# Performance work log

Hardware: AMD Instinct MI355X
Metric: run time of the kernel (lower is better)

Reference implementation:

```python
import math
import jax, jax.numpy as jnp
import numpy as np

D_MODEL = 1024
NUM_HEADS = 16
MAX_SEQ_LEN = 2048
THETA = 10000.0


def setup_inputs() -> dict:
    key = jax.random.key(0)
    ks = jax.random.split(key, 5)
    B, S, D = 2, 2048, D_MODEL
    std = math.sqrt(2.0 / (D + D))
    x = jax.random.normal(ks[0], (B, S, D), dtype=jnp.float32)
    wq = jax.random.normal(ks[1], (D, D), dtype=jnp.float32) * std
    wk = jax.random.normal(ks[2], (D, D), dtype=jnp.float32) * std
    wv = jax.random.normal(ks[3], (D, D), dtype=jnp.float32) * std
    wo = jax.random.normal(ks[4], (D, D), dtype=jnp.float32) * std
    return {"x": x, "wq": wq, "wk": wk, "wv": wv, "wo": wo}


def _rope_tables(seq_len: int, d_k: int):
    # angles[i, k] = i / theta^(2k/d_k), k over d_k//2 pairs
    inv_freq = 1.0 / (THETA ** (jnp.arange(0, d_k, 2, dtype=jnp.float32) / d_k))
    angles = jnp.arange(seq_len, dtype=jnp.float32)[:, None] * inv_freq[None, :]  # [S, d_k/2]
    return jnp.cos(angles), jnp.sin(angles)


def _apply_rope(x, cos, sin):
    # x: [..., S, d_k]; cos/sin: [S, d_k/2], broadcast over leading dims
    x_even = x[..., ::2]
    x_odd = x[..., 1::2]
    r_even = x_even * cos - x_odd * sin
    r_odd = x_even * sin + x_odd * cos
    return jnp.stack([r_even, r_odd], axis=-1).reshape(x.shape)


def reference(x, wq, wk, wv, wo):
    B, S, D = x.shape
    H = NUM_HEADS
    dk = D // H

    def split_heads(t):  # [B,S,D] -> [B,H,S,dk]
        return t.reshape(B, S, H, dk).transpose(0, 2, 1, 3)

    Q = split_heads(x @ wq.T)
    K = split_heads(x @ wk.T)
    V = split_heads(x @ wv.T)

    cos, sin = _rope_tables(S, dk)
    Q = _apply_rope(Q, cos, sin)
    K = _apply_rope(K, cos, sin)

    scores = jnp.einsum('bhqd,bhkd->bhqk', Q, K) / jnp.sqrt(jnp.float32(dk))
    mask = jnp.tril(jnp.ones((S, S), dtype=bool))  # causal: q can attend k <= q
    neg_inf = jnp.float32(-jnp.inf)
    scores = jnp.where(mask, scores, neg_inf)
    m = jnp.max(scores, axis=-1, keepdims=True)
    m = jnp.where(jnp.isinf(m), jnp.zeros_like(m), m)
    exp_scores = jnp.exp(scores - m)
    exp_scores = jnp.where(mask, exp_scores, 0.0)
    attn = exp_scores / (jnp.sum(exp_scores, axis=-1, keepdims=True) + 1e-9)
    out = jnp.einsum('bhqk,bhkd->bhqd', attn, V)  # [B,H,S,dk]
    out = out.transpose(0, 2, 1, 3).reshape(B, S, D)
    return out @ wo.T
```

## Files before the change

### kernel.cpp

```cpp
#include <hip/hip_runtime.h>
#include <stdint.h>

typedef unsigned short u16;
typedef unsigned int u32;
typedef __bf16 bf16x8 __attribute__((ext_vector_type(8)));
typedef float f32x4 __attribute__((ext_vector_type(4)));
typedef unsigned short u16x8 __attribute__((ext_vector_type(8)));

#define D_MODEL 1024
#define SEQ 2048
#define NH 16
#define DK 64
#define NROWS 4096

static __device__ __forceinline__ u16 f2bf(float f) {
  u32 u = __float_as_uint(f);
  u = (u + 0x7FFFu + ((u >> 16) & 1u)) >> 16;
  return (u16)u;
}
static __device__ __forceinline__ float bf2f(u16 h) {
  return __uint_as_float(((u32)h) << 16);
}
static __device__ __forceinline__ f32x4 mfma16(bf16x8 a, bf16x8 b, f32x4 c) {
  return __builtin_amdgcn_mfma_f32_16x16x32_bf16(a, b, c, 0, 0, 0);
}
static __device__ __forceinline__ void gload16(const void* g, void* l) {
  __builtin_amdgcn_global_load_lds(
      (const __attribute__((address_space(1))) void*)g,
      (__attribute__((address_space(3))) void*)l, 16, 0, 0);
}

static __device__ __forceinline__ float xor32_max(float x) {
#if __has_builtin(__builtin_amdgcn_permlane32_swap)
  u32 a = __float_as_uint(x), b = a;
  auto pr = __builtin_amdgcn_permlane32_swap(a, b, false, false);
  return fmaxf(__uint_as_float(pr[0]), __uint_as_float(pr[1]));
#else
  return fmaxf(x, __shfl_xor(x, 32));
#endif
}
static __device__ __forceinline__ float xor32_add(float x) {
#if __has_builtin(__builtin_amdgcn_permlane32_swap)
  u32 a = __float_as_uint(x), b = a;
  auto pr = __builtin_amdgcn_permlane32_swap(a, b, false, false);
  return __uint_as_float(pr[0]) + __uint_as_float(pr[1]);
#else
  return x + __shfl_xor(x, 32);
#endif
}

__global__ __launch_bounds__(256) void k_cast(
    const float* __restrict__ x, const float* __restrict__ wq,
    const float* __restrict__ wk, const float* __restrict__ wv,
    const float* __restrict__ wo, u16* __restrict__ xb, u16* __restrict__ wqb,
    u16* __restrict__ wkb, u16* __restrict__ wvb, u16* __restrict__ wob) {
  size_t e = ((size_t)blockIdx.x * 256 + threadIdx.x) * 8;
  const float* s;
  u16* d;
  size_t off;
  if (e < (size_t)NROWS * D_MODEL) {
    s = x; d = xb; off = e;
  } else {
    size_t r = e - (size_t)NROWS * D_MODEL;
    unsigned wi = (unsigned)(r >> 20);
    off = r & 1048575u;
    s = wi == 0 ? wq : wi == 1 ? wk : wi == 2 ? wv : wo;
    d = wi == 0 ? wqb : wi == 1 ? wkb : wi == 2 ? wvb : wob;
  }
  float4 a = *(const float4*)(s + off);
  float4 b = *(const float4*)(s + off + 4);
  u16x8 o;
  o[0] = f2bf(a.x); o[1] = f2bf(a.y); o[2] = f2bf(a.z); o[3] = f2bf(a.w);
  o[4] = f2bf(b.x); o[5] = f2bf(b.y); o[6] = f2bf(b.z); o[7] = f2bf(b.w);
  *(u16x8*)(d + off) = o;
}

__global__ __launch_bounds__(256) void k_tab(float* __restrict__ ct, float* __restrict__ st) {
  int i = blockIdx.x * 256 + threadIdx.x;
  int s = i >> 5, p = i & 31;
  double ang = (double)s * pow(10000.0, -(double)p / 32.0);
  ct[i] = (float)cos(ang);
  st[i] = (float)sin(ang);
}

template <bool MULTI, bool OUTF32>
__global__ __launch_bounds__(256, 1) void k_gemm(
    const u16* __restrict__ A, const u16* __restrict__ B0,
    const u16* __restrict__ B1, const u16* __restrict__ B2,
    u16* __restrict__ Cb, float* __restrict__ Cf, int ldc) {
  constexpr int K = 1024;
  const int mb = blockIdx.x, nb = blockIdx.y;
  const int tid = threadIdx.x;
  const int lane = tid & 63, w = tid >> 6;
  const int lq = lane & 15, lg = lane >> 4;
  const int wm = w >> 1, wn = w & 1;
  __shared__ __align__(16) u16 As[128 * 32];
  __shared__ __align__(16) u16 Bs[128 * 32];

  const u16* Bp;
  if (MULTI) {
    int sel = nb >> 3;
    Bp = sel == 0 ? B0 : (sel == 1 ? B1 : B2);
  } else {
    Bp = B0;
  }
  int nloc = MULTI ? (nb & 7) * 128 : nb * 128;
  const char* Ab = (const char*)A + (size_t)mb * 128 * 2048;
  const char* Bb = (const char*)Bp + (size_t)nloc * 2048;

  const int srow = tid >> 2;
  const int scb = (tid & 3) * 16;

  f32x4 zero4 = {0.f, 0.f, 0.f, 0.f};
  f32x4 acc[4][4];
#pragma unroll
  for (int i = 0; i < 4; ++i)
#pragma unroll
    for (int j = 0; j < 4; ++j) acc[i][j] = zero4;

  for (int k0 = 0; k0 < K; k0 += 32) {
#pragma unroll
    for (int c = 0; c < 2; ++c) {
      int o = c * 4096 + tid * 16;
      const char* ga = Ab + (size_t)(c * 64 + srow) * 2048 + k0 * 2 + scb;
      const char* gb = Bb + (size_t)(c * 64 + srow) * 2048 + k0 * 2 + scb;
      gload16(ga, (char*)As + o);
      gload16(gb, (char*)Bs + o);
    }
    __syncthreads();
    bf16x8 af[4], bfr[4];
#pragma unroll
    for (int i = 0; i < 4; ++i) {
      af[i] = *(const bf16x8*)((const char*)As + (wm * 64 + i * 16 + lq) * 64 + lg * 16);
      bfr[i] = *(const bf16x8*)((const char*)Bs + (wn * 64 + i * 16 + lq) * 64 + lg * 16);
    }
#pragma unroll
    for (int i = 0; i < 4; ++i)
#pragma unroll
      for (int j = 0; j < 4; ++j) acc[i][j] = mfma16(af[i], bfr[j], acc[i][j]);
    __syncthreads();
  }

#pragma unroll
  for (int i = 0; i < 4; ++i) {
#pragma unroll
    for (int r = 0; r < 4; ++r) {
      size_t rowg = (size_t)(mb * 128 + wm * 64 + i * 16 + lg * 4 + r);
#pragma unroll
      for (int j = 0; j < 4; ++j) {
        int colg = nb * 128 + wn * 64 + j * 16 + lq;
        if (OUTF32)
          Cf[rowg * ldc + colg] = acc[i][j][r];
        else
          Cb[rowg * ldc + colg] = f2bf(acc[i][j][r]);
      }
    }
  }
}

__global__ __launch_bounds__(256) void k_rope(const u16* __restrict__ qkv,
                                              const float* __restrict__ ct,
                                              const float* __restrict__ st,
                                              u16* __restrict__ qh, u16* __restrict__ kh) {
  int gi = blockIdx.x * 256 + threadIdx.x;
  int row = gi >> 7;
  int col = (gi & 127) << 3;
  int h = col >> 6, d0 = col & 63;
  int b = row >> 11, s = row & 2047;
  const int srcoff = blockIdx.y ? 1024 : 0;
  const float qs = blockIdx.y ? 1.0f : 0.18033688011112042f;
  u16x8 v = *(const u16x8*)(qkv + (size_t)row * 3072 + srcoff + col);
  const float* cp = ct + s * 32 + (d0 >> 1);
  const float* sp = st + s * 32 + (d0 >> 1);
  u16x8 o;
#pragma unroll
  for (int i = 0; i < 4; ++i) {
    float ev = bf2f(v[2 * i]), od = bf2f(v[2 * i + 1]);
    float c = cp[i], sn = sp[i];
    o[2 * i] = f2bf((ev * c - od * sn) * qs);
    o[2 * i + 1] = f2bf((ev * sn + od * c) * qs);
  }
  u16* dst = blockIdx.y ? kh : qh;
  *(u16x8*)(dst + (((size_t)(b * 16 + h) * SEQ + s) << 6) + d0) = o;
}

__global__ __launch_bounds__(256) void k_vtrans(const u16* __restrict__ qkv,
                                                u16* __restrict__ vt) {
  __shared__ __align__(16) u16 t[64][72];
  int sb = blockIdx.x, bh = blockIdx.y;
  int b = bh >> 4, h = bh & 15;
  int tid = threadIdx.x;
#pragma unroll
  for (int c = 0; c < 2; ++c) {
    int o = tid * 8 + c * 2048;
    int r = o >> 6, d = o & 63;
    u16x8 v = *(const u16x8*)(qkv + (size_t)(b * SEQ + sb * 64 + r) * 3072 + 2048 + h * 64 + d);
    *(u16x8*)&t[r][d] = v;
  }
  __syncthreads();
#pragma unroll
  for (int c = 0; c < 2; ++c) {
    int o = tid * 8 + c * 2048;
    int d = o >> 6, si = o & 63;
    u16x8 v;
#pragma unroll
    for (int j = 0; j < 8; ++j) v[j] = t[si + j][d];
    *(u16x8*)(vt + ((size_t)bh * 64 + d) * SEQ + sb * 64 + si) = v;
  }
}

static __device__ __forceinline__ void attn_tile(
    const u16* Kl, const u16* Vl, u16* Plw, int k0, int qrow, int lq, int lg,
    bf16x8 qf0, bf16x8 qf1, float& m_run, float& l_run, f32x4* accO, bool masked) {
  f32x4 zero4 = {0.f, 0.f, 0.f, 0.f};
  f32x4 sa[4];
  sa[0] = zero4; sa[1] = zero4; sa[2] = zero4; sa[3] = zero4;
  __builtin_amdgcn_s_setprio(1);
#pragma unroll
  for (int kt = 0; kt < 4; ++kt) {
    int krow = kt * 16 + lq;
    int base = krow * 128 + lg * 16;
    int swz = (krow & 7) << 4;
    bf16x8 kf0 = *(const bf16x8*)((const char*)Kl + (base ^ swz));
    bf16x8 kf1 = *(const bf16x8*)((const char*)Kl + ((base + 64) ^ swz));
    sa[kt] = mfma16(kf0, qf0, sa[kt]);
    sa[kt] = mfma16(kf1, qf1, sa[kt]);
  }
  __builtin_amdgcn_s_setprio(0);

  float p[16];
#pragma unroll
  for (int kt = 0; kt < 4; ++kt)
#pragma unroll
    for (int r = 0; r < 4; ++r) p[kt * 4 + r] = sa[kt][r];
  if (masked) {
#pragma unroll
    for (int kt = 0; kt < 4; ++kt)
#pragma unroll
      for (int r = 0; r < 4; ++r) {
        int key = k0 + kt * 16 + lg * 4 + r;
        if (key > qrow) p[kt * 4 + r] = -1e30f;
      }
  }
  float x0 = fmaxf(p[0], p[1]), x1 = fmaxf(p[2], p[3]);
  float x2 = fmaxf(p[4], p[5]), x3 = fmaxf(p[6], p[7]);
  float x4 = fmaxf(p[8], p[9]), x5 = fmaxf(p[10], p[11]);
  float x6 = fmaxf(p[12], p[13]), x7 = fmaxf(p[14], p[15]);
  x0 = fmaxf(x0, x1); x2 = fmaxf(x2, x3); x4 = fmaxf(x4, x5); x6 = fmaxf(x6, x7);
  x0 = fmaxf(x0, x2); x4 = fmaxf(x4, x6);
  float pm = fmaxf(x0, x4);
  pm = fmaxf(pm, __shfl_xor(pm, 16));
  pm = xor32_max(pm);
  const bool resc = __any(pm > m_run + 8.0f);
  float mnew = resc ? fmaxf(m_run, pm) : m_run;
#pragma unroll
  for (int i = 0; i < 16; ++i) p[i] = __builtin_amdgcn_exp2f(p[i] - mnew);
  float s0 = p[0] + p[1], s1 = p[2] + p[3], s2 = p[4] + p[5], s3 = p[6] + p[7];
  float s4 = p[8] + p[9], s5 = p[10] + p[11], s6 = p[12] + p[13], s7 = p[14] + p[15];
  s0 += s1; s2 += s3; s4 += s5; s6 += s7;
  s0 += s2; s4 += s6;
  float rs = s0 + s4;
  rs += __shfl_xor(rs, 16);
  rs = xor32_add(rs);
  if (resc) {
    float alpha = __builtin_amdgcn_exp2f(m_run - mnew);
    l_run = l_run * alpha + rs;
    m_run = mnew;
#pragma unroll
    for (int r = 0; r < 4; ++r) {
      float ar = __shfl(alpha, lg * 4 + r);
#pragma unroll
      for (int dt = 0; dt < 4; ++dt) accO[dt][r] *= ar;
    }
  } else {
    l_run += rs;
  }

  {
    int swz = (lq & 7) << 4;
#pragma unroll
    for (int kt = 0; kt < 4; ++kt) {
      u32 w0, w1;
      asm("v_cvt_pk_bf16_f32 %0, %1, %2"
          : "=v"(w0) : "v"(p[kt * 4 + 0]), "v"(p[kt * 4 + 1]));
      asm("v_cvt_pk_bf16_f32 %0, %1, %2"
          : "=v"(w1) : "v"(p[kt * 4 + 2]), "v"(p[kt * 4 + 3]));
      int a0 = (lq * 128 + (kt * 16 + lg * 4) * 2) ^ swz;
      int a1 = (lq * 128 + (kt * 16 + lg * 4 + 2) * 2) ^ swz;
      *(u32*)((char*)Plw + a0) = w0;
      *(u32*)((char*)Plw + a1) = w1;
    }
  }
  {
    int swz = (lq & 7) << 4;
    bf16x8 pa0 = *(const bf16x8*)((const char*)Plw + ((lq * 128 + lg * 16) ^ swz));
    bf16x8 pa1 = *(const bf16x8*)((const char*)Plw + ((lq * 128 + 64 + lg * 16) ^ swz));
    __builtin_amdgcn_s_setprio(1);
#pragma unroll
    for (int dt = 0; dt < 4; ++dt) {
      int vrow = dt * 16 + lq;
      int vb = vrow * 128 + lg * 16;
      int vs = (vrow & 7) << 4;
      bf16x8 v0 = *(const bf16x8*)((const char*)Vl + (vb ^ vs));
      bf16x8 v1 = *(const bf16x8*)((const char*)Vl + ((vb + 64) ^ vs));
      accO[dt] = mfma16(pa0, v0, accO[dt]);
      accO[dt] = mfma16(pa1, v1, accO[dt]);
    }
    __builtin_amdgcn_s_setprio(0);
  }
}

__global__ __launch_bounds__(512, 2) void k_attn(const u16* __restrict__ qh,
                                                 const u16* __restrict__ kh,
                                                 const u16* __restrict__ vt,
                                                 u16* __restrict__ ao) {
  const int qb1 = (int)blockIdx.x;
  const int qb2 = 15 - qb1;
  const int bh = blockIdx.y;
  const int tid = threadIdx.x;
  const int w = tid >> 6;
  const int lane = tid & 63;
  const int lq = lane & 15;
  const int lg = lane >> 4;

  __shared__ __align__(16) u16 Kd[2][64 * 64];
  __shared__ __align__(16) u16 Vd[2][64 * 64];
  __shared__ __align__(16) u16 Pl[8][16 * 64];

  const int qtop1 = qb1 * 128 + w * 16;
  const int qtop2 = qb2 * 128 + w * 16;
  const int qrow1 = qtop1 + lq;
  const int qrow2 = qtop2 + lq;

  const u16* qp1 = qh + ((size_t)bh * SEQ + qrow1) * DK + lg * 8;
  const u16* qp2 = qh + ((size_t)bh * SEQ + qrow2) * DK + lg * 8;
  bf16x8 qa0 = *(const bf16x8*)qp1;
  bf16x8 qa1 = *(const bf16x8*)(qp1 + 32);
  bf16x8 qb0 = *(const bf16x8*)qp2;
  bf16x8 qb1f = *(const bf16x8*)(qp2 + 32);

  f32x4 zero4 = {0.f, 0.f, 0.f, 0.f};
  f32x4 acc1[4], acc2[4];
#pragma unroll
  for (int dt = 0; dt < 4; ++dt) { acc1[dt] = zero4; acc2[dt] = zero4; }
  float m1 = -1e30f, l1 = 0.f, m2 = -1e30f, l2 = 0.f;

  const int NT = 2 * qb2 + 2;
  const int nt1 = 2 * qb1 + (w >> 2) + 1;
  const int nt2 = 2 * qb2 + (w >> 2) + 1;

  const int srow = tid >> 3;
  const int scb = (tid & 7) * 16;
  const int colb = scb ^ ((srow & 7) << 4);
  const char* kbase = (const char*)(kh + ((size_t)bh * SEQ + srow) * DK) + colb;
  const char* vbase = (const char*)(vt + ((size_t)bh * DK + srow) * SEQ) + colb;

  gload16(kbase, (char*)Kd[0] + tid * 16);
  gload16(vbase, (char*)Vd[0] + tid * 16);
  __syncthreads();

  for (int t = 0; t < NT; ++t) {
    const int cur = t & 1;
    if (t + 1 < NT) {
      gload16(kbase + (size_t)(t + 1) * 8192, (char*)Kd[cur ^ 1] + tid * 16);
      gload16(vbase + (size_t)(t + 1) * 128, (char*)Vd[cur ^ 1] + tid * 16);
    }
    const int k0 = t * 64;
    if (t < nt1)
      attn_tile(Kd[cur], Vd[cur], Pl[w], k0, qrow1, lq, lg, qa0, qa1, m1, l1,
                acc1, t == nt1 - 1);
    if (t < nt2)
      attn_tile(Kd[cur], Vd[cur], Pl[w], k0, qrow2, lq, lg, qb0, qb1f, m2, l2,
                acc2, t == nt2 - 1);
    __syncthreads();
  }

  const int b = bh >> 4, h = bh & 15;
#pragma unroll
  for (int r = 0; r < 4; ++r) {
    float lr = __shfl(l1, lg * 4 + r);
    float inv = 1.f / (lr + 1e-9f);
    int qq = qtop1 + lg * 4 + r;
    u16* orow = ao + ((size_t)b * SEQ + qq) * D_MODEL + h * DK;
#pragma unroll
    for (int dt = 0; dt < 4; ++dt) orow[dt * 16 + lq] = f2bf(acc1[dt][r] * inv);
  }
#pragma unroll
  for (int r = 0; r < 4; ++r) {
    float lr = __shfl(l2, lg * 4 + r);
    float inv = 1.f / (lr + 1e-9f);
    int qq = qtop2 + lg * 4 + r;
    u16* orow = ao + ((size_t)b * SEQ + qq) * D_MODEL + h * DK;
#pragma unroll
    for (int dt = 0; dt < 4; ++dt) orow[dt * 16 + lq] = f2bf(acc2[dt][r] * inv);
  }
}

extern "C" void kernel_launch(void* const* d_in, const int* in_sizes, int n_in,
                              void* d_out, int out_size, void* d_ws, size_t ws_size,
                              hipStream_t stream) {
  const float* x = (const float*)d_in[0];
  const float* wq = (const float*)d_in[1];
  const float* wk = (const float*)d_in[2];
  const float* wv = (const float*)d_in[3];
  const float* wo = (const float*)d_in[4];
  float* out = (float*)d_out;
  char* ws = (char*)d_ws;

  u16* xb   = (u16*)(ws + 0);
  u16* wqb  = (u16*)(ws + 8388608);
  u16* wkb  = (u16*)(ws + 10485760);
  u16* wvb  = (u16*)(ws + 12582912);
  u16* wob  = (u16*)(ws + 14680064);
  u16* qkv  = (u16*)(ws + 16777216);
  u16* qhb  = (u16*)(ws + 41943040);
  u16* khb  = (u16*)(ws + 50331648);
  u16* vtb  = (u16*)(ws + 58720256);
  u16* aob  = (u16*)(ws + 67108864);
  float* ct = (float*)(ws + 75497472);
  float* st = (float*)(ws + 75759616);

  k_cast<<<4096, 256, 0, stream>>>(x, wq, wk, wv, wo, xb, wqb, wkb, wvb, wob);
  k_tab<<<256, 256, 0, stream>>>(ct, st);
  k_gemm<true, false><<<dim3(32, 24), 256, 0, stream>>>(xb, wqb, wkb, wvb, qkv, nullptr, 3072);
  k_rope<<<dim3(2048, 2), 256, 0, stream>>>(qkv, ct, st, qhb, khb);
  k_vtrans<<<dim3(32, 32), 256, 0, stream>>>(qkv, vtb);
  k_attn<<<dim3(8, 32), 512, 0, stream>>>(qhb, khb, vtb, aob);
  k_gemm<false, true><<<dim3(32, 8), 256, 0, stream>>>(aob, wob, nullptr, nullptr, nullptr, out, 1024);
}
```

Baseline: 132.6 us.

## Shrink attention blocks to 64 query rows and stage two KV tiles per sync

The attention kernel now uses 256-thread blocks of four waves, each block covering two 64-row query tiles paired for causal load balance. The grid doubles to 16x32 blocks. Each loop iteration double-buffers and loads two 64-key K/V tiles, halving the number of __syncthreads per key range. The goal is more blocks for better CU occupancy and balance, and less barrier overhead. In exchange, K/V are loaded from global memory by more blocks, and per-block LDS use grows to about 72 KB.

```diff
diff --git a/kernel.cpp b/kernel.cpp
--- a/kernel.cpp
+++ b/kernel.cpp
@@ -310,12 +310,12 @@
   }
 }
 
-__global__ __launch_bounds__(512, 2) void k_attn(const u16* __restrict__ qh,
+__global__ __launch_bounds__(256, 2) void k_attn(const u16* __restrict__ qh,
                                                  const u16* __restrict__ kh,
                                                  const u16* __restrict__ vt,
                                                  u16* __restrict__ ao) {
   const int qb1 = (int)blockIdx.x;
-  const int qb2 = 15 - qb1;
+  const int qb2 = 31 - qb1;
   const int bh = blockIdx.y;
   const int tid = threadIdx.x;
   const int w = tid >> 6;
@@ -323,12 +323,12 @@
   const int lq = lane & 15;
   const int lg = lane >> 4;
 
-  __shared__ __align__(16) u16 Kd[2][64 * 64];
-  __shared__ __align__(16) u16 Vd[2][64 * 64];
-  __shared__ __align__(16) u16 Pl[8][16 * 64];
-
-  const int qtop1 = qb1 * 128 + w * 16;
-  const int qtop2 = qb2 * 128 + w * 16;
+  __shared__ __align__(16) u16 Kd[2][2][64 * 64];
+  __shared__ __align__(16) u16 Vd[2][2][64 * 64];
+  __shared__ __align__(16) u16 Pl[4][16 * 64];
+
+  const int qtop1 = qb1 * 64 + w * 16;
+  const int qtop2 = qb2 * 64 + w * 16;
   const int qrow1 = qtop1 + lq;
   const int qrow2 = qtop2 + lq;
 
@@ -336,8 +336,8 @@
   const u16* qp2 = qh + ((size_t)bh * SEQ + qrow2) * DK + lg * 8;
   bf16x8 qa0 = *(const bf16x8*)qp1;
   bf16x8 qa1 = *(const bf16x8*)(qp1 + 32);
-  bf16x8 qb0 = *(const bf16x8*)qp2;
-  bf16x8 qb1f = *(const bf16x8*)(qp2 + 32);
+  bf16x8 qc0 = *(const bf16x8*)qp2;
+  bf16x8 qc1 = *(const bf16x8*)(qp2 + 32);
 
   f32x4 zero4 = {0.f, 0.f, 0.f, 0.f};
   f32x4 acc1[4], acc2[4];
@@ -345,33 +345,55 @@
   for (int dt = 0; dt < 4; ++dt) { acc1[dt] = zero4; acc2[dt] = zero4; }
   float m1 = -1e30f, l1 = 0.f, m2 = -1e30f, l2 = 0.f;
 
-  const int NT = 2 * qb2 + 2;
-  const int nt1 = 2 * qb1 + (w >> 2) + 1;
-  const int nt2 = 2 * qb2 + (w >> 2) + 1;
-
-  const int srow = tid >> 3;
-  const int scb = (tid & 7) * 16;
-  const int colb = scb ^ ((srow & 7) << 4);
-  const char* kbase = (const char*)(kh + ((size_t)bh * SEQ + srow) * DK) + colb;
-  const char* vbase = (const char*)(vt + ((size_t)bh * DK + srow) * SEQ) + colb;
-
-  gload16(kbase, (char*)Kd[0] + tid * 16);
-  gload16(vbase, (char*)Vd[0] + tid * 16);
+  const int nt1 = qb1 + 1;
+  const int nt2 = qb2 + 1;
+  const int NIT = (nt2 + 1) >> 1;
+
+  const char* kb_ = (const char*)kh + (size_t)bh * SEQ * 128;
+  const char* vb_ = (const char*)vt + (size_t)bh * DK * 4096;
+
+#pragma unroll
+  for (int s = 0; s < 2; ++s)
+#pragma unroll
+    for (int pass = 0; pass < 2; ++pass) {
+      int chunk = pass * 256 + tid;
+      int srow = chunk >> 3;
+      int colb = ((chunk & 7) * 16) ^ ((srow & 7) << 4);
+      gload16(kb_ + (size_t)(s * 64 + srow) * 128 + colb,
+              (char*)Kd[0][s] + chunk * 16);
+      gload16(vb_ + (size_t)srow * 4096 + (s * 64) * 2 + colb,
+              (char*)Vd[0][s] + chunk * 16);
+    }
   __syncthreads();
 
-  for (int t = 0; t < NT; ++t) {
-    const int cur = t & 1;
-    if (t + 1 < NT) {
-      gload16(kbase + (size_t)(t + 1) * 8192, (char*)Kd[cur ^ 1] + tid * 16);
-      gload16(vbase + (size_t)(t + 1) * 128, (char*)Vd[cur ^ 1] + tid * 16);
-    }
-    const int k0 = t * 64;
-    if (t < nt1)
-      attn_tile(Kd[cur], Vd[cur], Pl[w], k0, qrow1, lq, lg, qa0, qa1, m1, l1,
-                acc1, t == nt1 - 1);
-    if (t < nt2)
-      attn_tile(Kd[cur], Vd[cur], Pl[w], k0, qrow2, lq, lg, qb0, qb1f, m2, l2,
-                acc2, t == nt2 - 1);
+  for (int it = 0; it < NIT; ++it) {
+    const int cur = it & 1;
+    if (it + 1 < NIT) {
+      int kb0 = (it + 1) * 128;
+#pragma unroll
+      for (int s = 0; s < 2; ++s)
+#pragma unroll
+        for (int pass = 0; pass < 2; ++pass) {
+          int chunk = pass * 256 + tid;
+          int srow = chunk >> 3;
+          int colb = ((chunk & 7) * 16) ^ ((srow & 7) << 4);
+          gload16(kb_ + (size_t)(kb0 + s * 64 + srow) * 128 + colb,
+                  (char*)Kd[cur ^ 1][s] + chunk * 16);
+          gload16(vb_ + (size_t)srow * 4096 + (kb0 + s * 64) * 2 + colb,
+                  (char*)Vd[cur ^ 1][s] + chunk * 16);
+        }
+    }
+#pragma unroll
+    for (int s = 0; s < 2; ++s) {
+      const int tsub = it * 2 + s;
+      const int k0 = tsub * 64;
+      if (tsub < nt1)
+        attn_tile(Kd[cur][s], Vd[cur][s], Pl[w], k0, qrow1, lq, lg, qa0, qa1,
+                  m1, l1, acc1, tsub == nt1 - 1);
+      if (tsub < nt2)
+        attn_tile(Kd[cur][s], Vd[cur][s], Pl[w], k0, qrow2, lq, lg, qc0, qc1,
+                  m2, l2, acc2, tsub == nt2 - 1);
+    }
     __syncthreads();
   }
 
@@ -425,6 +447,6 @@
   k_gemm<true, false><<<dim3(32, 24), 256, 0, stream>>>(xb, wqb, wkb, wvb, qkv, nullptr, 3072);
   k_rope<<<dim3(2048, 2), 256, 0, stream>>>(qkv, ct, st, qhb, khb);
   k_vtrans<<<dim3(32, 32), 256, 0, stream>>>(qkv, vtb);
-  k_attn<<<dim3(8, 32), 512, 0, stream>>>(qhb, khb, vtb, aob);
+  k_attn<<<dim3(16, 32), 256, 0, stream>>>(qhb, khb, vtb, aob);
   k_gemm<false, true><<<dim3(32, 8), 256, 0, stream>>>(aob, wob, nullptr, nullptr, nullptr, out, 1024);
 }
```

After: 126.2 us. -4.9%, faster.
